# Kernel tuning notes

Measured on AMD Instinct MI355X. Metric: run time of the kernel, lower is better.

Reference implementation:

```python
import jax, jax.numpy as jnp
import numpy as np
import math

D_MODEL = 1024
NUM_HEADS = 16
D_HEAD = D_MODEL // NUM_HEADS


def setup_inputs() -> dict:
    key = jax.random.key(0)
    ks = jax.random.split(key, 12)
    b, s = 2, 2048
    lim = 1.0 / math.sqrt(D_MODEL)
    def lin_w(k):
        return jax.random.uniform(k, (D_MODEL, D_MODEL), jnp.float32, -lim, lim)
    def lin_b(k):
        return jax.random.uniform(k, (D_MODEL,), jnp.float32, -lim, lim)
    return {
        "q": jax.random.normal(ks[0], (b, s, D_MODEL), jnp.float32),
        "k": jax.random.normal(ks[1], (b, s, D_MODEL), jnp.float32),
        "v": jax.random.normal(ks[2], (b, s, D_MODEL), jnp.float32),
        "mask": jax.random.randint(ks[3], (b, s, s), 0, 2, jnp.int32),
        "Wq": lin_w(ks[4]), "bq": lin_b(ks[5]),
        "Wk": lin_w(ks[6]), "bk": lin_b(ks[7]),
        "Wv": lin_w(ks[8]), "bv": lin_b(ks[9]),
        "Wo": lin_w(ks[10]), "bo": lin_b(ks[11]),
    }


def reference(q, k, v, mask, Wq, bq, Wk, bk, Wv, bv, Wo, bo):
    b, s, _ = q.shape
    h, dh = NUM_HEADS, D_HEAD
    # projections (torch Linear: x @ W.T + b), split heads -> (b, h, s, dh)
    qh = (q @ Wq.T + bq).reshape(b, s, h, dh).transpose(0, 2, 1, 3)
    kh = (k @ Wk.T + bk).reshape(b, s, h, dh).transpose(0, 2, 1, 3)
    vh = (v @ Wv.T + bv).reshape(b, s, h, dh).transpose(0, 2, 1, 3)
    # scaled dot-product scores (b, h, s_q, s_kv)
    scores = jnp.einsum("bhqd,bhkd->bhqk", qh, kh) / math.sqrt(dh)
    scores = jnp.where(mask[:, None, :, :] == 0, jnp.float32(-1e9), scores)
    score = jax.nn.softmax(scores, axis=-1)
    attn = jnp.einsum("bhqk,bhkd->bhqd", score, vh)  # (b, h, s, dh)
    # faithful to the torch code: raw reshape of (b, h, s, dh) -> (b, s, d_model)
    # WITHOUT transposing heads back (replicates the original's .view)
    out = attn.reshape(b, -1, D_MODEL) @ Wo.T + bo
    return out, score
```

## Files before the change

### kernel.cpp

```cpp
#include <hip/hip_runtime.h>

typedef __bf16 bf16_t;
typedef __bf16 bf16x4 __attribute__((ext_vector_type(4)));
typedef __bf16 bf16x8 __attribute__((ext_vector_type(8)));
typedef float f32x4 __attribute__((ext_vector_type(4)));

__device__ __forceinline__ void load_lds16(const void* g, void* l) {
    __builtin_amdgcn_global_load_lds((const __attribute__((address_space(1))) void*)g,
                                     (__attribute__((address_space(3))) void*)l, 16, 0, 0);
}

__global__ void cvt_all_k(const float* __restrict__ q, const float* __restrict__ k,
                          const float* __restrict__ v, const float* __restrict__ wq,
                          const float* __restrict__ wk, const float* __restrict__ wv,
                          const float* __restrict__ wo,
                          bf16_t* __restrict__ oq, bf16_t* __restrict__ ok,
                          bf16_t* __restrict__ ov, bf16_t* __restrict__ owq,
                          bf16_t* __restrict__ owk, bf16_t* __restrict__ owv,
                          bf16_t* __restrict__ owo) {
    int y = blockIdx.y;
    int n = (y < 3) ? 4194304 : 1048576;
    int i = (blockIdx.x * 256 + threadIdx.x) * 4;
    if (i >= n) return;
    const float* s;
    bf16_t* d;
    switch (y) {
        case 0: s = q;  d = oq;  break;
        case 1: s = k;  d = ok;  break;
        case 2: s = v;  d = ov;  break;
        case 3: s = wq; d = owq; break;
        case 4: s = wk; d = owk; break;
        case 5: s = wv; d = owv; break;
        default: s = wo; d = owo; break;
    }
    f32x4 t = *reinterpret_cast<const f32x4*>(s + i);
    *reinterpret_cast<bf16x4*>(d + i) = __builtin_convertvector(t, bf16x4);
}

__global__ void pack_mask_k(const int* __restrict__ mask, unsigned long long* __restrict__ bits) {
    int e = blockIdx.x * blockDim.x + threadIdx.x;
    unsigned long long b = __ballot(mask[e] != 0);
    if ((threadIdx.x & 63) == 0) bits[e >> 6] = b;
}

__global__ __launch_bounds__(256, 3) void gemm_qkv(
    const bf16_t* __restrict__ qb, const bf16_t* __restrict__ kb, const bf16_t* __restrict__ vb,
    const bf16_t* __restrict__ wq, const bf16_t* __restrict__ wk, const bf16_t* __restrict__ wv_,
    const float* __restrict__ bq, const float* __restrict__ bk, const float* __restrict__ bv,
    bf16_t* __restrict__ Qh, bf16_t* __restrict__ Kh, bf16_t* __restrict__ Vt)
{
    const int z = blockIdx.z;
    const bf16_t* A = (z == 0) ? qb : (z == 1) ? kb : vb;
    const bf16_t* W = (z == 0) ? wq : (z == 1) ? wk : wv_;
    const float* bias = (z == 0) ? bq : (z == 1) ? bk : bv;
    bf16_t* obf = (z == 0) ? Qh : (z == 1) ? Kh : Vt;

    __shared__ bf16_t As[128 * 64];
    __shared__ bf16_t Bs[128 * 64];
    const int tid = threadIdx.x;
    const int lane = tid & 63;
    const int wv = tid >> 6;
    const int wr = wv >> 1, wc = wv & 1;
    const int la = lane & 15, lb = lane >> 4;
    const int bRow = blockIdx.x, bCol = blockIdx.y;
    f32x4 acc[4][4] = {};

    for (int k0 = 0; k0 < 1024; k0 += 64) {
        __syncthreads();
        for (int i = 0; i < 4; ++i) {
            int o = i * 4096 + tid * 16;
            int row = o >> 7;
            int cb = (o & 127) ^ ((row & 7) << 4);
            const char* sa = (const char*)A + (((size_t)(bRow * 128 + row)) * 1024 + k0) * 2 + cb;
            load_lds16(sa, (char*)As + i * 4096 + wv * 1024);
            const char* sb = (const char*)W + (((size_t)(bCol * 128 + row)) * 1024 + k0) * 2 + cb;
            load_lds16(sb, (char*)Bs + i * 4096 + wv * 1024);
        }
        __syncthreads();

        bf16x8 af[2][4], bfr[2][4];
        for (int mi = 0; mi < 4; ++mi) {
            int row = wr * 64 + mi * 16 + la;
            const char* base = (const char*)As + row * 128;
            int sw = (row & 7) << 4;
            af[0][mi] = *reinterpret_cast<const bf16x8*>(base + ((lb * 16) ^ sw));
            af[1][mi] = *reinterpret_cast<const bf16x8*>(base + ((64 + lb * 16) ^ sw));
        }
        for (int ni = 0; ni < 4; ++ni) {
            int row = wc * 64 + ni * 16 + la;
            const char* base = (const char*)Bs + row * 128;
            int sw = (row & 7) << 4;
            bfr[0][ni] = *reinterpret_cast<const bf16x8*>(base + ((lb * 16) ^ sw));
            bfr[1][ni] = *reinterpret_cast<const bf16x8*>(base + ((64 + lb * 16) ^ sw));
        }
        for (int kk = 0; kk < 2; ++kk)
            for (int mi = 0; mi < 4; ++mi)
                for (int ni = 0; ni < 4; ++ni)
                    acc[mi][ni] = __builtin_amdgcn_mfma_f32_16x16x32_bf16(
                        af[kk][mi], bfr[kk][ni], acc[mi][ni], 0, 0, 0);
    }

    for (int ni = 0; ni < 4; ++ni) {
        int colo = bCol * 128 + wc * 64 + ni * 16 + la;
        float bvv = bias[colo];
        int h = colo >> 6, d = colo & 63;
        for (int mi = 0; mi < 4; ++mi) {
            int n0 = bRow * 128 + wr * 64 + mi * 16 + lb * 4;
            int b_ = n0 >> 11, s0 = n0 & 2047;
            if (z < 2) {
                for (int r = 0; r < 4; ++r) {
                    float v = acc[mi][ni][r] + bvv;
                    obf[(((size_t)(b_ * 16 + h) * 2048 + (s0 + r)) << 6) + d] = (bf16_t)v;
                }
            } else {
                f32x4 vv = acc[mi][ni];
                vv[0] += bvv; vv[1] += bvv; vv[2] += bvv; vv[3] += bvv;
                bf16x4 v4 = __builtin_convertvector(vv, bf16x4);
                *reinterpret_cast<bf16x4*>(
                    &obf[((size_t)(b_ * 16 + h) * 64 + d) * 2048 + s0]) = v4;
            }
        }
    }
}

__global__ __launch_bounds__(256, 3) void gemm_out(
    const bf16_t* __restrict__ A, const bf16_t* __restrict__ W,
    const float* __restrict__ bias, float* __restrict__ ofp)
{
    __shared__ bf16_t As[128 * 64];
    __shared__ bf16_t Bs[128 * 64];
    const int tid = threadIdx.x;
    const int lane = tid & 63;
    const int wv = tid >> 6;
    const int wr = wv >> 1, wc = wv & 1;
    const int la = lane & 15, lb = lane >> 4;
    const int bRow = blockIdx.x, bCol = blockIdx.y;
    f32x4 acc[4][4] = {};

    for (int k0 = 0; k0 < 1024; k0 += 64) {
        __syncthreads();
        for (int i = 0; i < 4; ++i) {
            int o = i * 4096 + tid * 16;
            int row = o >> 7;
            int cb = (o & 127) ^ ((row & 7) << 4);
            const char* sa = (const char*)A + (((size_t)(bRow * 128 + row)) * 1024 + k0) * 2 + cb;
            load_lds16(sa, (char*)As + i * 4096 + wv * 1024);
            const char* sb = (const char*)W + (((size_t)(bCol * 128 + row)) * 1024 + k0) * 2 + cb;
            load_lds16(sb, (char*)Bs + i * 4096 + wv * 1024);
        }
        __syncthreads();

        bf16x8 af[2][4], bfr[2][4];
        for (int mi = 0; mi < 4; ++mi) {
            int row = wr * 64 + mi * 16 + la;
            const char* base = (const char*)As + row * 128;
            int sw = (row & 7) << 4;
            af[0][mi] = *reinterpret_cast<const bf16x8*>(base + ((lb * 16) ^ sw));
            af[1][mi] = *reinterpret_cast<const bf16x8*>(base + ((64 + lb * 16) ^ sw));
        }
        for (int ni = 0; ni < 4; ++ni) {
            int row = wc * 64 + ni * 16 + la;
            const char* base = (const char*)Bs + row * 128;
            int sw = (row & 7) << 4;
            bfr[0][ni] = *reinterpret_cast<const bf16x8*>(base + ((lb * 16) ^ sw));
            bfr[1][ni] = *reinterpret_cast<const bf16x8*>(base + ((64 + lb * 16) ^ sw));
        }
        for (int kk = 0; kk < 2; ++kk)
            for (int mi = 0; mi < 4; ++mi)
                for (int ni = 0; ni < 4; ++ni)
                    acc[mi][ni] = __builtin_amdgcn_mfma_f32_16x16x32_bf16(
                        af[kk][mi], bfr[kk][ni], acc[mi][ni], 0, 0, 0);
    }

    for (int ni = 0; ni < 4; ++ni) {
        int colo = bCol * 128 + wc * 64 + ni * 16 + la;
        float bvv = bias[colo];
        for (int mi = 0; mi < 4; ++mi)
            for (int r = 0; r < 4; ++r) {
                int n = bRow * 128 + wr * 64 + mi * 16 + lb * 4 + r;
                __builtin_nontemporal_store(acc[mi][ni][r] + bvv,
                                            &ofp[(size_t)n * 1024 + colo]);
            }
    }
}

__global__ __launch_bounds__(512, 4) void attn_fused_k(
    const bf16_t* __restrict__ Qh, const bf16_t* __restrict__ Kh,
    const bf16_t* __restrict__ Vt, const unsigned int* __restrict__ mbits,
    float* __restrict__ P, bf16_t* __restrict__ attn)
{
    __shared__ bf16_t Ks[2][128 * 64];
    __shared__ bf16_t Pb[8][16 * 128];

    const int wg = blockIdx.x;
    const int swg = (wg & 7) * 64 + (wg >> 3);
    const int bh = swg >> 4, qs = swg & 15;

    const int tid = threadIdx.x, lane = tid & 63, wv = tid >> 6;
    const int la = lane & 15, lg = lane >> 4;
    const int b_ = bh >> 4;
    const int qbase = qs * 128 + wv * 16;
    const int swz = (la & 7) << 4;

    bf16x8 qf0, qf1;
    {
        const bf16_t* qrow = Qh + ((size_t)bh * 2048 + qbase + la) * 64 + lg * 8;
        qf0 = *reinterpret_cast<const bf16x8*>(qrow);
        qf1 = *reinterpret_cast<const bf16x8*>(qrow + 32);
    }
    const char* Khb = (const char*)(Kh + ((size_t)bh << 17));
    const bf16_t* Vtb = Vt + ((size_t)bh << 17);
    const unsigned int* mrow = mbits + ((size_t)b_ * 2048 + qbase + la) * 64;
    const float SC = 0.125f * 1.4426950408889634f;

#define STAGE_K(c, bsel)                                                      \
    for (int i = 0; i < 2; ++i) {                                             \
        int o = i * 8192 + tid * 16;                                          \
        int row = o >> 7;                                                     \
        int cb = (o & 127) ^ ((row & 7) << 4);                                \
        load_lds16(Khb + (size_t)(c) * 16384 + row * 128 + cb,                \
                   (char*)Ks[bsel] + i * 8192 + wv * 1024);                   \
    }

    float ssum = 0.f;
    uint4 mws = *reinterpret_cast<const uint4*>(mrow);
    STAGE_K(0, 0)
    __syncthreads();
    for (int c = 0; c < 16; ++c) {
        int cn = (c < 15) ? c + 1 : 15;
        uint4 mnext = *reinterpret_cast<const uint4*>(mrow + cn * 4);
        if (c < 15) { STAGE_K(c + 1, (c + 1) & 1) }
        __builtin_amdgcn_sched_barrier(0);
        const char* Kbase = (const char*)Ks[c & 1];
        unsigned mwarr[4] = {mws.x, mws.y, mws.z, mws.w};
        __builtin_amdgcn_s_setprio(1);
#pragma unroll
        for (int ct = 0; ct < 8; ++ct) {
            int krow = ct * 16 + la;
            const char* kb = Kbase + krow * 128;
            int sw = (krow & 7) << 4;
            bf16x8 kf0 = *reinterpret_cast<const bf16x8*>(kb + ((lg * 16) ^ sw));
            bf16x8 kf1 = *reinterpret_cast<const bf16x8*>(kb + ((64 + lg * 16) ^ sw));
            f32x4 acc = {};
            acc = __builtin_amdgcn_mfma_f32_16x16x32_bf16(kf0, qf0, acc, 0, 0, 0);
            acc = __builtin_amdgcn_mfma_f32_16x16x32_bf16(kf1, qf1, acc, 0, 0, 0);
            unsigned mw = mwarr[ct >> 1];
            int shift = ((ct & 1) << 4) + lg * 4;
            for (int r = 0; r < 4; ++r) {
                float t = __builtin_amdgcn_exp2f(acc[r] * SC);
                ssum += ((mw >> (shift + r)) & 1u) ? t : 0.f;
            }
        }
        __builtin_amdgcn_s_setprio(0);
        __syncthreads();
        mws = mnext;
    }
    ssum += __shfl_xor(ssum, 16, 64);
    ssum += __shfl_xor(ssum, 32, 64);
    const float nls = -__builtin_amdgcn_logf(ssum);

    f32x4 accpv[4] = {};
    float* Pq = P + ((size_t)bh << 22) + (size_t)(qbase + la) * 2048;
    char* Pw = (char*)Pb[wv];
    mws = *reinterpret_cast<const uint4*>(mrow);
    STAGE_K(0, 0)
    __syncthreads();
    for (int c = 0; c < 16; ++c) {
        int cn = (c < 15) ? c + 1 : 15;
        uint4 mnext = *reinterpret_cast<const uint4*>(mrow + cn * 4);
        if (c < 15) { STAGE_K(c + 1, (c + 1) & 1) }
        __builtin_amdgcn_sched_barrier(0);
        const char* Kbase = (const char*)Ks[c & 1];
        unsigned mwarr[4] = {mws.x, mws.y, mws.z, mws.w};
        __builtin_amdgcn_s_setprio(1);
#pragma unroll
        for (int ct = 0; ct < 8; ++ct) {
            int krow = ct * 16 + la;
            const char* kb = Kbase + krow * 128;
            int sw = (krow & 7) << 4;
            bf16x8 kf0 = *reinterpret_cast<const bf16x8*>(kb + ((lg * 16) ^ sw));
            bf16x8 kf1 = *reinterpret_cast<const bf16x8*>(kb + ((64 + lg * 16) ^ sw));
            f32x4 acc = {};
            acc = __builtin_amdgcn_mfma_f32_16x16x32_bf16(kf0, qf0, acc, 0, 0, 0);
            acc = __builtin_amdgcn_mfma_f32_16x16x32_bf16(kf1, qf1, acc, 0, 0, 0);
            unsigned mw = mwarr[ct >> 1];
            int shift = ((ct & 1) << 4) + lg * 4;
            f32x4 pv;
            for (int r = 0; r < 4; ++r) {
                float t = __builtin_amdgcn_exp2f(__builtin_fmaf(acc[r], SC, nls));
                pv[r] = ((mw >> (shift + r)) & 1u) ? t : 0.f;
            }
            __builtin_nontemporal_store(
                pv, reinterpret_cast<f32x4*>(Pq + c * 128 + ct * 16 + lg * 4));
            bf16x4 pb4 = __builtin_convertvector(pv, bf16x4);
            *reinterpret_cast<bf16x4*>(Pw + ((la * 256 + ct * 32 + lg * 8) ^ swz)) = pb4;
        }
        asm volatile("s_waitcnt lgkmcnt(0)" ::: "memory");
        __builtin_amdgcn_sched_barrier(0);
        for (int kbk = 0; kbk < 4; ++kbk) {
            bf16x8 pa = *reinterpret_cast<const bf16x8*>(
                Pw + ((la * 256 + kbk * 64 + lg * 16) ^ swz));
            const bf16_t* vb2 = Vtb + c * 128 + kbk * 32 + lg * 8;
            for (int ni = 0; ni < 4; ++ni) {
                bf16x8 vf = *reinterpret_cast<const bf16x8*>(vb2 + (size_t)(ni * 16 + la) * 2048);
                accpv[ni] = __builtin_amdgcn_mfma_f32_16x16x32_bf16(pa, vf, accpv[ni], 0, 0, 0);
            }
        }
        __builtin_amdgcn_s_setprio(0);
        asm volatile("s_waitcnt vmcnt(8)" ::: "memory");
        __builtin_amdgcn_s_barrier();
        mws = mnext;
    }
#undef STAGE_K

    bf16_t* ab = attn + ((size_t)bh << 17);
    for (int ni = 0; ni < 4; ++ni)
        for (int r = 0; r < 4; ++r)
            ab[(size_t)(qbase + lg * 4 + r) * 64 + ni * 16 + la] = (bf16_t)accpv[ni][r];
}

extern "C" void kernel_launch(void* const* d_in, const int* in_sizes, int n_in,
                              void* d_out, int out_size, void* d_ws, size_t ws_size,
                              hipStream_t stream) {
    const float* q  = (const float*)d_in[0];
    const float* k  = (const float*)d_in[1];
    const float* v  = (const float*)d_in[2];
    const int* mask = (const int*)d_in[3];
    const float* Wq = (const float*)d_in[4];
    const float* bq = (const float*)d_in[5];
    const float* Wk = (const float*)d_in[6];
    const float* bk = (const float*)d_in[7];
    const float* Wv = (const float*)d_in[8];
    const float* bv = (const float*)d_in[9];
    const float* Wo = (const float*)d_in[10];
    const float* bo = (const float*)d_in[11];

    char* ws = (char*)d_ws;
    bf16_t* qb    = (bf16_t*)(ws + 0);
    bf16_t* kb    = (bf16_t*)(ws + 8388608);
    bf16_t* vb    = (bf16_t*)(ws + 16777216);
    bf16_t* wqb   = (bf16_t*)(ws + 25165824);
    bf16_t* wkb   = (bf16_t*)(ws + 27262976);
    bf16_t* wvb   = (bf16_t*)(ws + 29360128);
    bf16_t* wob   = (bf16_t*)(ws + 31457280);
    bf16_t* Qh    = (bf16_t*)(ws + 33554432);
    bf16_t* Kh    = (bf16_t*)(ws + 41943040);
    bf16_t* Vt    = (bf16_t*)(ws + 50331648);
    bf16_t* attnb = (bf16_t*)(ws + 58720256);
    unsigned long long* mbits = (unsigned long long*)(ws + 67108864);

    float* out   = (float*)d_out;
    float* score = out + 4194304;

    cvt_all_k<<<dim3(4096, 7), 256, 0, stream>>>(q, k, v, Wq, Wk, Wv, Wo,
                                                 qb, kb, vb, wqb, wkb, wvb, wob);
    pack_mask_k<<<32768, 256, 0, stream>>>(mask, mbits);

    gemm_qkv<<<dim3(32, 8, 3), 256, 0, stream>>>(qb, kb, vb, wqb, wkb, wvb,
                                                 bq, bk, bv, Qh, Kh, Vt);

    attn_fused_k<<<512, 512, 0, stream>>>(Qh, Kh, Vt, (const unsigned int*)mbits,
                                          score, attnb);

    gemm_out<<<dim3(32, 8), 256, 0, stream>>>(attnb, wob, bo, out);
}
```

Before: 298.7 us.

## Load K fragments directly from global memory instead of LDS double-buffering

Result: slower. 463.0 us (+55.0%).

```diff
diff --git a/kernel.cpp b/kernel.cpp
--- a/kernel.cpp
+++ b/kernel.cpp
@@ -189,7 +189,6 @@
     const bf16_t* __restrict__ Vt, const unsigned int* __restrict__ mbits,
     float* __restrict__ P, bf16_t* __restrict__ attn)
 {
-    __shared__ bf16_t Ks[2][128 * 64];
     __shared__ bf16_t Pb[8][16 * 128];
 
     const int wg = blockIdx.x;
@@ -213,34 +212,15 @@
     const unsigned int* mrow = mbits + ((size_t)b_ * 2048 + qbase + la) * 64;
     const float SC = 0.125f * 1.4426950408889634f;
 
-#define STAGE_K(c, bsel)                                                      \
-    for (int i = 0; i < 2; ++i) {                                             \
-        int o = i * 8192 + tid * 16;                                          \
-        int row = o >> 7;                                                     \
-        int cb = (o & 127) ^ ((row & 7) << 4);                                \
-        load_lds16(Khb + (size_t)(c) * 16384 + row * 128 + cb,                \
-                   (char*)Ks[bsel] + i * 8192 + wv * 1024);                   \
-    }
-
     float ssum = 0.f;
-    uint4 mws = *reinterpret_cast<const uint4*>(mrow);
-    STAGE_K(0, 0)
-    __syncthreads();
     for (int c = 0; c < 16; ++c) {
-        int cn = (c < 15) ? c + 1 : 15;
-        uint4 mnext = *reinterpret_cast<const uint4*>(mrow + cn * 4);
-        if (c < 15) { STAGE_K(c + 1, (c + 1) & 1) }
-        __builtin_amdgcn_sched_barrier(0);
-        const char* Kbase = (const char*)Ks[c & 1];
+        uint4 mws = *reinterpret_cast<const uint4*>(mrow + c * 4);
         unsigned mwarr[4] = {mws.x, mws.y, mws.z, mws.w};
-        __builtin_amdgcn_s_setprio(1);
 #pragma unroll
         for (int ct = 0; ct < 8; ++ct) {
-            int krow = ct * 16 + la;
-            const char* kb = Kbase + krow * 128;
-            int sw = (krow & 7) << 4;
-            bf16x8 kf0 = *reinterpret_cast<const bf16x8*>(kb + ((lg * 16) ^ sw));
-            bf16x8 kf1 = *reinterpret_cast<const bf16x8*>(kb + ((64 + lg * 16) ^ sw));
+            const char* kb = Khb + (size_t)(c * 128 + ct * 16 + la) * 128 + lg * 16;
+            bf16x8 kf0 = *reinterpret_cast<const bf16x8*>(kb);
+            bf16x8 kf1 = *reinterpret_cast<const bf16x8*>(kb + 64);
             f32x4 acc = {};
             acc = __builtin_amdgcn_mfma_f32_16x16x32_bf16(kf0, qf0, acc, 0, 0, 0);
             acc = __builtin_amdgcn_mfma_f32_16x16x32_bf16(kf1, qf1, acc, 0, 0, 0);
@@ -251,9 +231,6 @@
                 ssum += ((mw >> (shift + r)) & 1u) ? t : 0.f;
             }
         }
-        __builtin_amdgcn_s_setprio(0);
-        __syncthreads();
-        mws = mnext;
     }
     ssum += __shfl_xor(ssum, 16, 64);
     ssum += __shfl_xor(ssum, 32, 64);
@@ -262,24 +239,14 @@
     f32x4 accpv[4] = {};
     float* Pq = P + ((size_t)bh << 22) + (size_t)(qbase + la) * 2048;
     char* Pw = (char*)Pb[wv];
-    mws = *reinterpret_cast<const uint4*>(mrow);
-    STAGE_K(0, 0)
-    __syncthreads();
     for (int c = 0; c < 16; ++c) {
-        int cn = (c < 15) ? c + 1 : 15;
-        uint4 mnext = *reinterpret_cast<const uint4*>(mrow + cn * 4);
-        if (c < 15) { STAGE_K(c + 1, (c + 1) & 1) }
-        __builtin_amdgcn_sched_barrier(0);
-        const char* Kbase = (const char*)Ks[c & 1];
+        uint4 mws = *reinterpret_cast<const uint4*>(mrow + c * 4);
         unsigned mwarr[4] = {mws.x, mws.y, mws.z, mws.w};
-        __builtin_amdgcn_s_setprio(1);
 #pragma unroll
         for (int ct = 0; ct < 8; ++ct) {
-            int krow = ct * 16 + la;
-            const char* kb = Kbase + krow * 128;
-            int sw = (krow & 7) << 4;
-            bf16x8 kf0 = *reinterpret_cast<const bf16x8*>(kb + ((lg * 16) ^ sw));
-            bf16x8 kf1 = *reinterpret_cast<const bf16x8*>(kb + ((64 + lg * 16) ^ sw));
+            const char* kb = Khb + (size_t)(c * 128 + ct * 16 + la) * 128 + lg * 16;
+            bf16x8 kf0 = *reinterpret_cast<const bf16x8*>(kb);
+            bf16x8 kf1 = *reinterpret_cast<const bf16x8*>(kb + 64);
             f32x4 acc = {};
             acc = __builtin_amdgcn_mfma_f32_16x16x32_bf16(kf0, qf0, acc, 0, 0, 0);
             acc = __builtin_amdgcn_mfma_f32_16x16x32_bf16(kf1, qf1, acc, 0, 0, 0);
@@ -306,12 +273,7 @@
                 accpv[ni] = __builtin_amdgcn_mfma_f32_16x16x32_bf16(pa, vf, accpv[ni], 0, 0, 0);
             }
         }
-        __builtin_amdgcn_s_setprio(0);
-        asm volatile("s_waitcnt vmcnt(8)" ::: "memory");
-        __builtin_amdgcn_s_barrier();
-        mws = mnext;
-    }
-#undef STAGE_K
+    }
 
     bf16_t* ab = attn + ((size_t)bh << 17);
     for (int ni = 0; ni < 4; ++ni)
```
